# Kernel tuning notes

Hardware: AMD Instinct MI355X
Metric: run time of the kernel (lower is better)

## Reference

```python
import jax, jax.numpy as jnp
import numpy as np

DIM = 128
HEADS = 4
DIM_HEAD = 32
HIDDEN = HEADS * DIM_HEAD  # 128
EPS = 1e-5


def setup_inputs() -> dict:
    key = jax.random.key(0)
    ks = jax.random.split(key, 5)
    x = jax.random.normal(ks[0], (32, DIM, 64, 64), dtype=jnp.float32)
    # 1x1 convs are channel matmuls
    Wqkv = jax.random.normal(ks[1], (HIDDEN * 3, DIM), dtype=jnp.float32) * (1.0 / np.sqrt(DIM))
    Wout = jax.random.normal(ks[2], (DIM, HIDDEN), dtype=jnp.float32) * (1.0 / np.sqrt(HIDDEN))
    bout = jnp.zeros((DIM,), dtype=jnp.float32)
    ln_w = jnp.ones((DIM,), dtype=jnp.float32)
    ln_b = jnp.zeros((DIM,), dtype=jnp.float32)
    return {"x": x, "Wqkv": Wqkv, "Wout": Wout, "bout": bout, "ln_w": ln_w, "ln_b": ln_b}


def reference(x, Wqkv, Wout, bout, ln_w, ln_b):
    b, c, h, w = x.shape
    n = h * w
    xf = x.reshape(b, c, n)  # b c n
    qkv = jnp.einsum('oc,bcn->bon', Wqkv, xf)  # b (3*hidden) n
    q, k, v = jnp.split(qkv, 3, axis=1)
    # b (h d) n -> b h d n
    q = q.reshape(b, HEADS, DIM_HEAD, n)
    k = k.reshape(b, HEADS, DIM_HEAD, n)
    v = v.reshape(b, HEADS, DIM_HEAD, n)
    q = jax.nn.softmax(q, axis=-2)  # over feature dim d
    k = jax.nn.softmax(k, axis=-1)  # over spatial dim n
    context = jnp.einsum('bhdn,bhen->bhde', k, v)
    out = jnp.einsum('bhde,bhdn->bhen', context, q)  # b h e n
    out = out.reshape(b, HIDDEN, n)
    out = jnp.einsum('oc,bcn->bon', Wout, out) + bout[None, :, None]
    out = out.reshape(b, DIM, h, w)
    # LayerNorm2d over channel dim, biased variance
    mean = jnp.mean(out, axis=1, keepdims=True)
    var = jnp.var(out, axis=1, keepdims=True)
    out = (out - mean) / jnp.sqrt(var + EPS) * ln_w[None, :, None, None] + ln_b[None, :, None, None]
    return out
```

## Files before the change

kernel.cpp:

```cpp
#include <hip/hip_runtime.h>
#include <stdint.h>


constexpr int B_   = 32;
constexpr int C_   = 128;
constexpr int N_   = 4096;
constexpr int O3_  = 384;
constexpr int NSUB = 8;
constexpr int TPB_ = 8;

using short8  = __attribute__((ext_vector_type(8))) short;
using short4v = __attribute__((ext_vector_type(4))) short;
using float4v = __attribute__((ext_vector_type(4))) float;

__device__ __forceinline__ unsigned short bf16_rne(float f) {
    union { float f; uint32_t u; } v; v.f = f;
    uint32_t u = v.u;
    u += 0x7FFFu + ((u >> 16) & 1u);
    return (unsigned short)(u >> 16);
}
__device__ __forceinline__ float bf2f(unsigned short h) {
    union { uint32_t u; float f; } v; v.u = ((uint32_t)h) << 16; return v.f;
}

constexpr size_t OFF_WQ   = 0;
constexpr size_t OFF_WO   = 98304;
constexpr size_t OFF_SP   = 131072;
constexpr size_t OFF_CTXP = 393216;
constexpr size_t OFF_CTXN = 8781824;
constexpr size_t OFF_QSM  = 9043968;

__global__ __launch_bounds__(256) void k0_prep(const float* __restrict__ Wqkv,
                                               const float* __restrict__ Wout,
                                               unsigned short* __restrict__ wq,
                                               unsigned short* __restrict__ wo) {
    int t = blockIdx.x * 256 + threadIdx.x;
    if (t < O3_ * C_) wq[t] = bf16_rne(Wqkv[t]);
    if (t < C_ * C_)  wo[t] = bf16_rne(Wout[t]);
}

__global__ __launch_bounds__(1024) void k1_qkv(const float* __restrict__ x,
                                               const unsigned short* __restrict__ wq,
                                               unsigned short* __restrict__ qsm,
                                               float* __restrict__ ctx_part,
                                               float* __restrict__ S_part) {
    __shared__ __align__(16) unsigned short xs0[64 * 136];
    __shared__ __align__(16) unsigned short xs1[64 * 136];
    __shared__ __align__(16) unsigned short ek[128 * 72];
    __shared__ __align__(16) unsigned short vsh[128 * 72];

    const int b    = blockIdx.y;
    const int tblk = blockIdx.x;
    const int tid  = threadIdx.x;

    const int lane = tid & 63;
    const int wv   = tid >> 6;
    const int l15  = lane & 15;
    const int quad = lane >> 4;

    const float4v zero = {0.f, 0.f, 0.f, 0.f};

    short8 wfa[8];
    if (wv < 12) {
        const unsigned short* wqp = wq + (wv * 32 + l15) * C_ + quad * 8;
        #pragma unroll
        for (int kk = 0; kk < 4; kk++) {
            wfa[kk]     = *(const short8*)(wqp + kk * 32);
            wfa[4 + kk] = *(const short8*)(wqp + 16 * C_ + kk * 32);
        }
    }

    const int sid = tid & 255;
    const int snl = sid & 63;
    const int scg = sid >> 6;
    const float* xbase = x + ((size_t)b * C_ + (size_t)scg * 32) * N_ + snl;
    float xv[32];
    auto load_x = [&](int s) {
        const float* xp = xbase + (tblk * NSUB + s) * 64;
        #pragma unroll
        for (int i = 0; i < 32; i++) xv[i] = xp[(size_t)i * N_];
    };
    auto store_x = [&](unsigned short* xs) {
        unsigned short* dst = &xs[snl * 136 + scg * 32];
        #pragma unroll
        for (int ii = 0; ii < 4; ii++) {
            short8 v8;
            #pragma unroll
            for (int j = 0; j < 8; j++) v8[j] = (short)bf16_rne(xv[ii * 8 + j]);
            *(short8*)(dst + ii * 8) = v8;
        }
    };

    if (wv >= 12) { load_x(0); store_x(xs0); }
    unsigned short* xs_cur = xs0;
    unsigned short* xs_nxt = xs1;

    float4v cacc = zero;
    float s_acc  = 0.f;
    const int ch  = wv >> 2;
    const int cdt = (wv >> 1) & 1;
    const int cet = wv & 1;

    for (int s = 0; s < NSUB; s++) {
        const int ns = (tblk * NSUB + s) * 64;
        __syncthreads();

        if (wv < 12) {
            #pragma unroll
            for (int ct = 0; ct < 4; ct++) {
                short8 bfx[4];
                #pragma unroll
                for (int kk = 0; kk < 4; kk++)
                    bfx[kk] = *(const short8*)&xs_cur[(ct * 16 + l15) * 136 + kk * 32 + quad * 8];
                float4v acc0 = zero, acc1 = zero;
                #pragma unroll
                for (int kk = 0; kk < 4; kk++) {
                    acc0 = __builtin_amdgcn_mfma_f32_16x16x32_bf16(wfa[kk],     bfx[kk], acc0, 0, 0, 0);
                    acc1 = __builtin_amdgcn_mfma_f32_16x16x32_bf16(wfa[4 + kk], bfx[kk], acc1, 0, 0, 0);
                }
                const int ncol = ct * 16 + l15;
                if (wv < 4) {
                    float e0[4], e1[4], z = 0.f;
                    #pragma unroll
                    for (int r = 0; r < 4; r++) {
                        e0[r] = __expf(acc0[r]); e1[r] = __expf(acc1[r]);
                        z += e0[r] + e1[r];
                    }
                    z += __shfl_xor(z, 16, 64);
                    z += __shfl_xor(z, 32, 64);
                    const float iz = 1.0f / z;
                    unsigned short* qp = qsm + ((size_t)b * N_ + ns + ncol) * C_ + wv * 32 + quad * 4;
                    short4v s0, s1;
                    #pragma unroll
                    for (int r = 0; r < 4; r++) {
                        s0[r] = (short)bf16_rne(e0[r] * iz);
                        s1[r] = (short)bf16_rne(e1[r] * iz);
                    }
                    *(short4v*)qp = s0;
                    *(short4v*)(qp + 16) = s1;
                } else if (wv < 8) {
                    const int row0 = (wv - 4) * 32 + quad * 4;
                    #pragma unroll
                    for (int r = 0; r < 4; r++) {
                        ek[(row0 + r) * 72 + ncol]      = bf16_rne(__expf(acc0[r]));
                        ek[(row0 + 16 + r) * 72 + ncol] = bf16_rne(__expf(acc1[r]));
                    }
                } else {
                    const int row0 = (wv - 8) * 32 + quad * 4;
                    #pragma unroll
                    for (int r = 0; r < 4; r++) {
                        vsh[(row0 + r) * 72 + ncol]      = bf16_rne(acc0[r]);
                        vsh[(row0 + 16 + r) * 72 + ncol] = bf16_rne(acc1[r]);
                    }
                }
            }
        } else {
            if (s + 1 < NSUB) { load_x(s + 1); store_x(xs_nxt); }
        }
        __syncthreads();

        {
            const unsigned short* ap = &ek[(ch * 32 + cdt * 16 + l15) * 72 + quad * 8];
            const unsigned short* bp = &vsh[(ch * 32 + cet * 16 + l15) * 72 + quad * 8];
            #pragma unroll
            for (int kk = 0; kk < 2; kk++) {
                short8 a  = *(const short8*)(ap + kk * 32);
                short8 bb = *(const short8*)(bp + kk * 32);
                cacc = __builtin_amdgcn_mfma_f32_16x16x32_bf16(a, bb, cacc, 0, 0, 0);
            }
        }
        {
            const unsigned short* ep = &ek[(tid >> 3) * 72 + (tid & 7) * 8];
            short8 e0 = *(const short8*)ep;
            float ss = 0.f;
            #pragma unroll
            for (int j = 0; j < 8; j++) ss += bf2f((unsigned short)e0[j]);
            s_acc += ss;
        }
        { unsigned short* t = xs_cur; xs_cur = xs_nxt; xs_nxt = t; }
    }

    {
        float* cp = ctx_part + ((size_t)(b * TPB_ + tblk) << 12)
                  + ((ch * 32 + cdt * 16 + quad * 4) * 32 + cet * 16 + l15);
        #pragma unroll
        for (int r = 0; r < 4; r++) cp[r * 32] = cacc[r];
    }
    {
        float ss = s_acc;
        ss += __shfl_xor(ss, 1, 64);
        ss += __shfl_xor(ss, 2, 64);
        ss += __shfl_xor(ss, 4, 64);
        if ((tid & 7) == 0)
            S_part[(size_t)(b * TPB_ + tblk) * 128 + (tid >> 3)] = ss;
    }
}

__global__ __launch_bounds__(256) void k2_reduce(const float* __restrict__ ctx_part,
                                                 const float* __restrict__ S_part,
                                                 unsigned short* __restrict__ ctxn) {
    __shared__ float Sinv[128];
    const int b     = blockIdx.x >> 3;
    const int chunk = blockIdx.x & 7;
    const int tid   = threadIdx.x;
    if (tid < 128) {
        float s = 0.f;
        #pragma unroll
        for (int t = 0; t < TPB_; t++)
            s += S_part[(size_t)(b * TPB_ + t) * 128 + tid];
        Sinv[tid] = 1.0f / s;
    }
    __syncthreads();
    #pragma unroll
    for (int j = 0; j < 2; j++) {
        const int ei = chunk * 512 + j * 256 + tid;
        float v = 0.f;
        #pragma unroll
        for (int t = 0; t < TPB_; t++)
            v += ctx_part[((size_t)(b * TPB_ + t) << 12) + ei];
        const int h = ei >> 10, d = (ei >> 5) & 31, e = ei & 31;
        ctxn[(size_t)b * 4096 + (h * 32 + e) * 32 + d] = bf16_rne(v * Sinv[h * 32 + d]);
    }
}

__global__ __launch_bounds__(256) void k3_out(const unsigned short* __restrict__ qsm,
                                              const unsigned short* __restrict__ ctxn,
                                              const unsigned short* __restrict__ wo,
                                              const float* __restrict__ bout,
                                              const float* __restrict__ lnw,
                                              const float* __restrict__ lnb,
                                              float* __restrict__ out) {
    __shared__ __align__(16) unsigned short o2[64 * 136];

    const int b  = blockIdx.y;
    const int n0 = blockIdx.x * 64;
    const int tid = threadIdx.x;

    const int lane = tid & 63, wv = tid >> 6, l15 = lane & 15, quad = lane >> 4;
    const int nl = wv * 16 + l15;
    const size_t n = (size_t)n0 + nl;

    const float4v zero = {0.f, 0.f, 0.f, 0.f};

    short8 bq[4], ca[4][2];
    #pragma unroll
    for (int h = 0; h < 4; h++)
        bq[h] = *(const short8*)(qsm + ((size_t)b * N_ + n) * C_ + h * 32 + quad * 8);
    #pragma unroll
    for (int h = 0; h < 4; h++)
        #pragma unroll
        for (int et = 0; et < 2; et++)
            ca[h][et] = *(const short8*)(ctxn + (size_t)b * 4096 + (h * 32 + et * 16 + l15) * 32 + quad * 8);

    #pragma unroll
    for (int h = 0; h < 4; h++) {
        #pragma unroll
        for (int et = 0; et < 2; et++) {
            float4v c4 = __builtin_amdgcn_mfma_f32_16x16x32_bf16(ca[h][et], bq[h], zero, 0, 0, 0);
            short4v s4;
            #pragma unroll
            for (int r = 0; r < 4; r++) s4[r] = (short)bf16_rne(c4[r]);
            *(short4v*)&o2[nl * 136 + h * 32 + et * 16 + quad * 4] = s4;
        }
    }
    __syncthreads();

    short8 bfr[4];
    #pragma unroll
    for (int kk = 0; kk < 4; kk++)
        bfr[kk] = *(const short8*)&o2[nl * 136 + kk * 32 + quad * 8];

    float4v acc[8];
    #pragma unroll
    for (int ot = 0; ot < 8; ot++) {
        const unsigned short* wp = wo + (ot * 16 + l15) * C_ + quad * 8;
        short8 w[4];
        #pragma unroll
        for (int kk = 0; kk < 4; kk++) w[kk] = *(const short8*)(wp + kk * 32);
        acc[ot] = zero;
        #pragma unroll
        for (int kk = 0; kk < 4; kk++)
            acc[ot] = __builtin_amdgcn_mfma_f32_16x16x32_bf16(w[kk], bfr[kk], acc[ot], 0, 0, 0);
    }

    float sum = 0.f, sq = 0.f;
    #pragma unroll
    for (int ot = 0; ot < 8; ot++) {
        #pragma unroll
        for (int r = 0; r < 4; r++) {
            const int o = ot * 16 + quad * 4 + r;
            const float y = acc[ot][r] + bout[o];
            acc[ot][r] = y;
            sum += y; sq += y * y;
        }
    }
    sum += __shfl_xor(sum, 16, 64);
    sum += __shfl_xor(sum, 32, 64);
    sq  += __shfl_xor(sq, 16, 64);
    sq  += __shfl_xor(sq, 32, 64);
    const float mean = sum * (1.0f / 128.0f);
    const float var  = sq * (1.0f / 128.0f) - mean * mean;
    const float rstd = rsqrtf(var + 1e-5f);

    #pragma unroll
    for (int ot = 0; ot < 8; ot++) {
        #pragma unroll
        for (int r = 0; r < 4; r++) {
            const int o = ot * 16 + quad * 4 + r;
            out[((size_t)b * C_ + o) * N_ + n] = (acc[ot][r] - mean) * rstd * lnw[o] + lnb[o];
        }
    }
}

extern "C" void kernel_launch(void* const* d_in, const int* in_sizes, int n_in,
                              void* d_out, int out_size, void* d_ws, size_t ws_size,
                              hipStream_t stream) {
    const float* x    = (const float*)d_in[0];
    const float* Wqkv = (const float*)d_in[1];
    const float* Wout = (const float*)d_in[2];
    const float* bout = (const float*)d_in[3];
    const float* lnw  = (const float*)d_in[4];
    const float* lnb  = (const float*)d_in[5];
    float* out = (float*)d_out;

    char* ws = (char*)d_ws;
    unsigned short* wq   = (unsigned short*)(ws + OFF_WQ);
    unsigned short* wo   = (unsigned short*)(ws + OFF_WO);
    float* S_part        = (float*)(ws + OFF_SP);
    float* ctx_part      = (float*)(ws + OFF_CTXP);
    unsigned short* ctxn = (unsigned short*)(ws + OFF_CTXN);
    unsigned short* qsm  = (unsigned short*)(ws + OFF_QSM);

    k0_prep<<<192, 256, 0, stream>>>(Wqkv, Wout, wq, wo);
    k1_qkv<<<dim3(TPB_, B_), 1024, 0, stream>>>(x, wq, qsm, ctx_part, S_part);
    k2_reduce<<<B_ * 8, 256, 0, stream>>>(ctx_part, S_part, ctxn);
    k3_out<<<dim3(N_ / 64, B_), 256, 0, stream>>>(qsm, ctxn, wo, bout, lnw, lnb, out);
}
```

Before: 181.2 us.

## Fold normalized context into output projection as per-batch weight matrix

The reduce kernel now multiplies Wout by the normalized context matrix once per batch, producing a per-batch fused 128x128 weight. The output kernel then applies a single GEMM to the softmaxed queries instead of two chained MFMA stages with an LDS round trip and a barrier. This removes per-tile work in the hot output kernel. In exchange the reduce kernel launches only one block per batch, so it has less parallelism, and the fused weight adds an extra bf16 rounding.

```diff
diff --git a/kernel.cpp b/kernel.cpp
--- a/kernel.cpp
+++ b/kernel.cpp
@@ -26,9 +26,9 @@
 constexpr size_t OFF_WQ   = 0;
 constexpr size_t OFF_WO   = 98304;
 constexpr size_t OFF_SP   = 131072;
-constexpr size_t OFF_CTXP = 393216;
-constexpr size_t OFF_CTXN = 8781824;
-constexpr size_t OFF_QSM  = 9043968;
+constexpr size_t OFF_CTXP = 262144;
+constexpr size_t OFF_WBIG = 4456448;
+constexpr size_t OFF_QSM  = 5505024;
 
 __global__ __launch_bounds__(256) void k0_prep(const float* __restrict__ Wqkv,
                                                const float* __restrict__ Wout,
@@ -196,13 +196,15 @@
     }
 }
 
-__global__ __launch_bounds__(256) void k2_reduce(const float* __restrict__ ctx_part,
+__global__ __launch_bounds__(512) void k2_reduce(const float* __restrict__ ctx_part,
                                                  const float* __restrict__ S_part,
-                                                 unsigned short* __restrict__ ctxn) {
+                                                 const unsigned short* __restrict__ wo,
+                                                 unsigned short* __restrict__ wbig) {
     __shared__ float Sinv[128];
-    const int b     = blockIdx.x >> 3;
-    const int chunk = blockIdx.x & 7;
-    const int tid   = threadIdx.x;
+    __shared__ __align__(16) unsigned short ctxb[128 * 40];
+    const int b   = blockIdx.x;
+    const int tid = threadIdx.x;
+
     if (tid < 128) {
         float s = 0.f;
         #pragma unroll
@@ -211,29 +213,41 @@
         Sinv[tid] = 1.0f / s;
     }
     __syncthreads();
-    #pragma unroll
-    for (int j = 0; j < 2; j++) {
-        const int ei = chunk * 512 + j * 256 + tid;
+
+    #pragma unroll
+    for (int i = 0; i < 8; i++) {
+        const int ei = i * 512 + tid;
         float v = 0.f;
         #pragma unroll
         for (int t = 0; t < TPB_; t++)
             v += ctx_part[((size_t)(b * TPB_ + t) << 12) + ei];
-        const int h = ei >> 10, d = (ei >> 5) & 31, e = ei & 31;
-        ctxn[(size_t)b * 4096 + (h * 32 + e) * 32 + d] = bf16_rne(v * Sinv[h * 32 + d]);
+        ctxb[(ei >> 5) * 40 + (ei & 31)] = bf16_rne(v * Sinv[ei >> 5]);
+    }
+    __syncthreads();
+
+    const int lane = tid & 63, wv = tid >> 6, l15 = lane & 15, quad = lane >> 4;
+    const float4v zero = {0.f, 0.f, 0.f, 0.f};
+    unsigned short* wb = wbig + (size_t)b * (C_ * C_);
+    #pragma unroll
+    for (int ht = 0; ht < 8; ht++) {
+        const int h_ = ht >> 1;
+        short8 a  = *(const short8*)(wo + (wv * 16 + l15) * C_ + h_ * 32 + quad * 8);
+        short8 bb = *(const short8*)&ctxb[(h_ * 32 + (ht & 1) * 16 + l15) * 40 + quad * 8];
+        float4v c4 = __builtin_amdgcn_mfma_f32_16x16x32_bf16(a, bb, zero, 0, 0, 0);
+        #pragma unroll
+        for (int r = 0; r < 4; r++)
+            wb[(wv * 16 + quad * 4 + r) * C_ + ht * 16 + l15] = bf16_rne(c4[r]);
     }
 }
 
 __global__ __launch_bounds__(256) void k3_out(const unsigned short* __restrict__ qsm,
-                                              const unsigned short* __restrict__ ctxn,
-                                              const unsigned short* __restrict__ wo,
+                                              const unsigned short* __restrict__ wbig,
                                               const float* __restrict__ bout,
                                               const float* __restrict__ lnw,
                                               const float* __restrict__ lnb,
                                               float* __restrict__ out) {
-    __shared__ __align__(16) unsigned short o2[64 * 136];
-
-    const int b  = blockIdx.y;
-    const int n0 = blockIdx.x * 64;
+    const int b   = blockIdx.y;
+    const int n0  = blockIdx.x * 64;
     const int tid = threadIdx.x;
 
     const int lane = tid & 63, wv = tid >> 6, l15 = lane & 15, quad = lane >> 4;
@@ -242,45 +256,26 @@
 
     const float4v zero = {0.f, 0.f, 0.f, 0.f};
 
-    short8 bq[4], ca[4][2];
-    #pragma unroll
-    for (int h = 0; h < 4; h++)
-        bq[h] = *(const short8*)(qsm + ((size_t)b * N_ + n) * C_ + h * 32 + quad * 8);
-    #pragma unroll
-    for (int h = 0; h < 4; h++)
-        #pragma unroll
-        for (int et = 0; et < 2; et++)
-            ca[h][et] = *(const short8*)(ctxn + (size_t)b * 4096 + (h * 32 + et * 16 + l15) * 32 + quad * 8);
-
-    #pragma unroll
-    for (int h = 0; h < 4; h++) {
-        #pragma unroll
-        for (int et = 0; et < 2; et++) {
-            float4v c4 = __builtin_amdgcn_mfma_f32_16x16x32_bf16(ca[h][et], bq[h], zero, 0, 0, 0);
-            short4v s4;
-            #pragma unroll
-            for (int r = 0; r < 4; r++) s4[r] = (short)bf16_rne(c4[r]);
-            *(short4v*)&o2[nl * 136 + h * 32 + et * 16 + quad * 4] = s4;
-        }
-    }
-    __syncthreads();
-
-    short8 bfr[4];
+    short8 bq[4];
     #pragma unroll
     for (int kk = 0; kk < 4; kk++)
-        bfr[kk] = *(const short8*)&o2[nl * 136 + kk * 32 + quad * 8];
-
+        bq[kk] = *(const short8*)(qsm + ((size_t)b * N_ + n) * C_ + kk * 32 + quad * 8);
+
+    const unsigned short* wbp = wbig + (size_t)b * (C_ * C_);
     float4v acc[8];
     #pragma unroll
     for (int ot = 0; ot < 8; ot++) {
-        const unsigned short* wp = wo + (ot * 16 + l15) * C_ + quad * 8;
-        short8 w[4];
-        #pragma unroll
-        for (int kk = 0; kk < 4; kk++) w[kk] = *(const short8*)(wp + kk * 32);
-        acc[ot] = zero;
-        #pragma unroll
-        for (int kk = 0; kk < 4; kk++)
-            acc[ot] = __builtin_amdgcn_mfma_f32_16x16x32_bf16(w[kk], bfr[kk], acc[ot], 0, 0, 0);
+        const unsigned short* wp = wbp + (ot * 16 + l15) * C_ + quad * 8;
+        short8 w0 = *(const short8*)(wp);
+        short8 w1 = *(const short8*)(wp + 32);
+        short8 w2 = *(const short8*)(wp + 64);
+        short8 w3 = *(const short8*)(wp + 96);
+        float4v a = zero;
+        a = __builtin_amdgcn_mfma_f32_16x16x32_bf16(w0, bq[0], a, 0, 0, 0);
+        a = __builtin_amdgcn_mfma_f32_16x16x32_bf16(w1, bq[1], a, 0, 0, 0);
+        a = __builtin_amdgcn_mfma_f32_16x16x32_bf16(w2, bq[2], a, 0, 0, 0);
+        a = __builtin_amdgcn_mfma_f32_16x16x32_bf16(w3, bq[3], a, 0, 0, 0);
+        acc[ot] = a;
     }
 
     float sum = 0.f, sq = 0.f;
@@ -328,11 +323,11 @@
     unsigned short* wo   = (unsigned short*)(ws + OFF_WO);
     float* S_part        = (float*)(ws + OFF_SP);
     float* ctx_part      = (float*)(ws + OFF_CTXP);
-    unsigned short* ctxn = (unsigned short*)(ws + OFF_CTXN);
+    unsigned short* wbig = (unsigned short*)(ws + OFF_WBIG);
     unsigned short* qsm  = (unsigned short*)(ws + OFF_QSM);
 
     k0_prep<<<192, 256, 0, stream>>>(Wqkv, Wout, wq, wo);
     k1_qkv<<<dim3(TPB_, B_), 1024, 0, stream>>>(x, wq, qsm, ctx_part, S_part);
-    k2_reduce<<<B_ * 8, 256, 0, stream>>>(ctx_part, S_part, ctxn);
-    k3_out<<<dim3(N_ / 64, B_), 256, 0, stream>>>(qsm, ctxn, wo, bout, lnw, lnb, out);
-}
+    k2_reduce<<<B_, 512, 0, stream>>>(ctx_part, S_part, wo, wbig);
+    k3_out<<<dim3(N_ / 64, B_), 256, 0, stream>>>(qsm, wbig, bout, lnw, lnb, out);
+}
```

Result: faster. 177.7 us (-2.0%).
